# Kernel optimization log

Measured on AMD Instinct MI355X. Metric: run time of the kernel, lower is better.

The kernel has to match this reference:

```python
import jax, jax.numpy as jnp
import numpy as np

BATCH, T, N = 8, 2048, 512


def setup_inputs() -> dict:
    key = jax.random.key(0)
    ks = jax.random.split(key, 8)
    scale = 1.0 / np.sqrt(2.0 * (N + N) / 2.0) / np.sqrt(2.0)  # GlorotNormal / sqrt(2)
    u = jax.random.normal(ks[0], (BATCH, T, N), dtype=jnp.float32)
    C_re = jax.random.normal(ks[1], (N, N), dtype=jnp.float32) * scale
    C_im = jax.random.normal(ks[2], (N, N), dtype=jnp.float32) * scale
    B_re = jax.random.normal(ks[3], (N, N), dtype=jnp.float32) * scale
    B_im = jax.random.normal(ks[4], (N, N), dtype=jnp.float32) * scale
    D = jax.random.normal(ks[5], (N,), dtype=jnp.float32)
    # nu drawn from the numerically-stable end of [log(-log rmax), log(-log rmin)]
    nu = jax.random.uniform(ks[6], (N,), minval=-4.6, maxval=-3.7, dtype=jnp.float32)
    theta = jax.random.uniform(ks[7], (N,), minval=0.0, maxval=3.14 / 10, dtype=jnp.float32)
    # gamma initialized as sqrt(1 - |lambda|^2), lambda = exp(-exp(nu) + i*theta)
    gamma = jnp.sqrt(1.0 - jnp.exp(-2.0 * jnp.exp(nu)))
    return {"u": u, "C_re": C_re, "C_im": C_im, "B_re": B_re, "B_im": B_im,
            "D": D, "nu": nu, "theta": theta, "gamma": gamma}


def reference(u, C_re, C_im, B_re, B_im, D, nu, theta, gamma):
    # log_lambda = -exp(nu) + i*theta  (the TF code names this `lambda_`)
    log_lam = (-jnp.exp(nu)).astype(jnp.complex64) + 1j * theta.astype(jnp.complex64)  # (n,)
    t = jnp.arange(u.shape[1], dtype=jnp.float32).astype(jnp.complex64)[:, None]       # (T,1)
    lam_pow = jnp.exp(log_lam[None, :] * t)    # (T,n) == diag(Lambda^t)
    lam_minpow = jnp.exp(-log_lam[None, :] * t)  # (T,n) == diag(Lambda^-t)
    Bm = (B_re + 1j * B_im).astype(jnp.complex64)  # (n,n)
    Cm = (C_re + 1j * C_im).astype(jnp.complex64)  # (n,n)
    # new_u = (gamma * u) @ B   (complex)
    new_u = (gamma * u).astype(jnp.complex64) @ Bm  # (b,t,n)
    # diag einsums in the original are elementwise multiplies
    x = jnp.cumsum(new_u * lam_minpow[None], axis=1) * lam_pow[None]  # (b,t,n)
    y = jnp.real(x @ Cm) + D * u
    return y
```

## Files before the change

kernel.cpp:

```cpp
#include <hip/hip_runtime.h>
#include <hip/hip_bf16.h>
#include <math.h>
#include <stdint.h>

#define BATCH 8
#define T_LEN 2048
#define NDIM 512
#define M_ROWS (BATCH * T_LEN)
#define CHUNK 32
#define NCHUNK (T_LEN / CHUNK)


typedef __attribute__((ext_vector_type(8))) short bf16x8;
typedef __attribute__((ext_vector_type(4))) float floatx4;

__device__ __forceinline__ unsigned short f2bf(float f) {
    union { float f; unsigned u; } v; v.f = f;
    unsigned r = v.u + 0x7fff + ((v.u >> 16) & 1);
    return (unsigned short)(r >> 16);
}
__device__ __forceinline__ float bf2f(unsigned short h) {
    union { unsigned u; float f; } v; v.u = ((unsigned)h) << 16;
    return v.f;
}
__device__ __forceinline__ float bf2f_lo(unsigned u) {
    union { unsigned u; float f; } v; v.u = u << 16; return v.f;
}
__device__ __forceinline__ float bf2f_hi(unsigned u) {
    union { unsigned u; float f; } v; v.u = u & 0xffff0000u; return v.f;
}

__device__ __forceinline__ void gld_lds16(const unsigned short* g, unsigned short* l) {
    __builtin_amdgcn_global_load_lds(
        (const __attribute__((address_space(1))) unsigned int*)(uintptr_t)g,
        (__attribute__((address_space(3))) unsigned int*)(uintptr_t)l,
        16, 0, 0);
}

__global__ __launch_bounds__(256) void k_prep(
    const float* __restrict__ u,
    const float* __restrict__ Bre, const float* __restrict__ Bim,
    const float* __restrict__ Cre, const float* __restrict__ Cim,
    const float* __restrict__ gamma,
    unsigned short* __restrict__ ubf,
    unsigned short* __restrict__ BT, unsigned short* __restrict__ CT)
{
    __shared__ unsigned short tile[32][33];
    const int blk = blockIdx.x;
    if (blk < 4096) {
        size_t i = ((size_t)blk * 256 + threadIdx.x) * 8;
        float4 a = *(const float4*)&u[i];
        float4 b = *(const float4*)&u[i + 4];
        ushort4 p0, p1;
        p0.x = f2bf(a.x); p0.y = f2bf(a.y); p0.z = f2bf(a.z); p0.w = f2bf(a.w);
        p1.x = f2bf(b.x); p1.y = f2bf(b.y); p1.z = f2bf(b.z); p1.w = f2bf(b.w);
        *(ushort4*)&ubf[i] = p0;
        *(ushort4*)&ubf[i + 4] = p1;
        return;
    }
    const int p = blk - 4096;
    const int z = p >> 8;
    const int rem = p & 255;
    const int n0 = (rem & 15) * 32, k0 = (rem >> 4) * 32;
    const float* __restrict__ src = (z == 0) ? Bre : (z == 1) ? Bim : (z == 2) ? Cre : Cim;
    const int tx = threadIdx.x & 31, ty = threadIdx.x >> 5;

#pragma unroll
    for (int j = 0; j < 4; ++j) {
        int k = k0 + ty + j * 8;
        float s = (z < 2) ? gamma[k] : (z == 3 ? -1.f : 1.f);
        tile[ty + j * 8][tx] = f2bf(s * src[(size_t)k * NDIM + n0 + tx]);
    }
    __syncthreads();
#pragma unroll
    for (int j = 0; j < 4; ++j) {
        int n = n0 + ty + j * 8;
        unsigned short v = tile[tx][ty + j * 8];
        if (z == 0) {
            int row = ((n >> 6) << 7) + (n & 63);
            BT[(size_t)row * 512 + k0 + tx] = v;
        } else if (z == 1) {
            int row = ((n >> 6) << 7) + 64 + (n & 63);
            BT[(size_t)row * 512 + k0 + tx] = v;
        } else if (z == 2) {
            int k = k0 + tx;
            int col = ((k >> 6) << 7) + (k & 63);
            CT[(size_t)n * 1024 + col] = v;
        } else {
            int k = k0 + tx;
            int col = ((k >> 6) << 7) + 64 + (k & 63);
            CT[(size_t)n * 1024 + col] = v;
        }
    }
}

__global__ __launch_bounds__(256) void k_gemm_in(
    const unsigned short* __restrict__ A,
    const unsigned short* __restrict__ BT,
    const float* __restrict__ nu, const float* __restrict__ theta,
    unsigned short* __restrict__ X,
    float* __restrict__ carry)
{
    __shared__ unsigned short smem[16384];
    unsigned short* const As0 = smem;
    unsigned short* const As1 = smem + 4096;
    unsigned short* const Bs0 = smem + 8192;
    unsigned short* const Bs1 = smem + 12288;

    const int tid = threadIdx.x;
    const int w = tid >> 6, l = tid & 63;
    const int bm = blockIdx.x * 128;
    const int bn = blockIdx.y * 128;
    const int wm = (w & 1) * 64, wn = (w >> 1) * 64;
    const int lm = l & 15, lq = l >> 4;
    const int srow = w * 16 + (l >> 2);
    const int scol = (l & 3) * 8;

    floatx4 acc[4][4];
#pragma unroll
    for (int i = 0; i < 4; ++i)
#pragma unroll
        for (int j = 0; j < 4; ++j) acc[i][j] = (floatx4)0.f;

    auto STAGE = [&](unsigned short* as, unsigned short* bs, int k0) {
        gld_lds16(&A[(size_t)(bm + srow) * 512 + k0 + scol],       &as[srow * 32 + scol]);
        gld_lds16(&A[(size_t)(bm + 64 + srow) * 512 + k0 + scol],  &as[(64 + srow) * 32 + scol]);
        gld_lds16(&BT[(size_t)(bn + srow) * 512 + k0 + scol],      &bs[srow * 32 + scol]);
        gld_lds16(&BT[(size_t)(bn + 64 + srow) * 512 + k0 + scol], &bs[(64 + srow) * 32 + scol]);
    };
    auto COMPUTE = [&](const unsigned short* as, const unsigned short* bs) {
        bf16x8 af[4], bfr[4];
#pragma unroll
        for (int i = 0; i < 4; ++i)
            af[i] = *(const bf16x8*)&as[(wm + i * 16 + lm) * 32 + lq * 8];
#pragma unroll
        for (int j = 0; j < 4; ++j)
            bfr[j] = *(const bf16x8*)&bs[(wn + j * 16 + lm) * 32 + lq * 8];
#pragma unroll
        for (int i = 0; i < 4; ++i)
#pragma unroll
            for (int j = 0; j < 4; ++j)
                acc[i][j] = __builtin_amdgcn_mfma_f32_16x16x32_bf16(af[i], bfr[j], acc[i][j], 0, 0, 0);
    };

    STAGE(As0, Bs0, 0);
    __syncthreads();
#pragma unroll
    for (int k0 = 0; k0 < 512; k0 += 64) {
        if (k0 + 32 < 512) STAGE(As1, Bs1, k0 + 32);
        COMPUTE(As0, Bs0);
        __syncthreads();
        if (k0 + 64 < 512) STAGE(As0, Bs0, k0 + 64);
        COMPUTE(As1, Bs1);
        __syncthreads();
    }

#pragma unroll
    for (int i = 0; i < 4; ++i)
#pragma unroll
        for (int j = 0; j < 4; ++j) {
            int col = wn + j * 16 + lm;
#pragma unroll
            for (int r = 0; r < 4; ++r) {
                int row = wm + i * 16 + lq * 4 + r;
                unsigned short v = f2bf(acc[i][j][r]);
                smem[row * 128 + col] = v;
                X[(size_t)(bm + row) * 1024 + bn + col] = v;
            }
        }
    __syncthreads();
    {
        const int chunk = tid >> 6;
        const int ch = tid & 63;
        const int n = (bn >> 1) + ch;
        const float rr = __expf(-__expf(nu[n]));
        const float lre = rr * __cosf(theta[n]);
        const float lim = rr * __sinf(theta[n]);
        const unsigned short* base = &smem[chunk * 32 * 128 + ch];
        float xre = 0.f, xim = 0.f;
#pragma unroll 8
        for (int t = 0; t < 32; ++t) {
            float ure = bf2f(base[t * 128]);
            float uim = bf2f(base[t * 128 + 64]);
            float a = lre * xre - lim * xim + ure;
            float b = lre * xim + lim * xre + uim;
            xre = a; xim = b;
        }
        const int bb = bm >> 11;
        const int cg = ((bm & 2047) >> 5) + chunk;
        size_t ci = ((size_t)bb * NCHUNK + cg) * NDIM + n;
        *(float2*)&carry[ci * 2] = make_float2(xre, xim);
    }
}

__global__ __launch_bounds__(256) void k_scan_apply(
    unsigned short* __restrict__ X,
    const float* __restrict__ nu, const float* __restrict__ theta,
    const float* __restrict__ carry)
{
    const int t2 = threadIdx.x;
    const int n0 = 2 * t2;
    const int b = blockIdx.x >> 6, c = blockIdx.x & 63;
    const float ex0 = __expf(nu[n0]), ex1 = __expf(nu[n0 + 1]);
    const float r0 = __expf(-ex0), r1 = __expf(-ex1);
    const float lre0 = r0 * __cosf(theta[n0]),     lim0 = r0 * __sinf(theta[n0]);
    const float lre1 = r1 * __cosf(theta[n0 + 1]), lim1 = r1 * __sinf(theta[n0 + 1]);
    const float rc0 = expf(-ex0 * (float)CHUNK), rc1 = expf(-ex1 * (float)CHUNK);
    const float th0 = theta[n0] * (float)CHUNK,  th1 = theta[n0 + 1] * (float)CHUNK;
    const float A0 = rc0 * cosf(th0), B0 = rc0 * sinf(th0);
    const float A1 = rc1 * cosf(th1), B1 = rc1 * sinf(th1);

    float xre0 = 0.f, xim0 = 0.f, xre1 = 0.f, xim1 = 0.f;
    for (int cc = 0; cc < c; ++cc) {
        size_t idx = ((size_t)b * NCHUNK + cc) * NDIM + n0;
        float4 cv = *(const float4*)&carry[idx * 2];
        float a0 = A0 * xre0 - B0 * xim0 + cv.x;
        float b0 = A0 * xim0 + B0 * xre0 + cv.y;
        float a1 = A1 * xre1 - B1 * xim1 + cv.z;
        float b1 = A1 * xim1 + B1 * xre1 + cv.w;
        xre0 = a0; xim0 = b0; xre1 = a1; xim1 = b1;
    }

    const int recol = ((n0 >> 6) << 7) + (n0 & 63);
    size_t m = (size_t)b * T_LEN + (size_t)c * CHUNK;
#pragma unroll 8
    for (int t = 0; t < CHUNK; ++t, ++m) {
        unsigned re = *(const unsigned*)&X[m * 1024 + recol];
        unsigned im = *(const unsigned*)&X[m * 1024 + recol + 64];
        float u0 = bf2f_lo(re), u1 = bf2f_hi(re);
        float v0 = bf2f_lo(im), v1 = bf2f_hi(im);
        float a0 = lre0 * xre0 - lim0 * xim0 + u0;
        float b0 = lre0 * xim0 + lim0 * xre0 + v0;
        float a1 = lre1 * xre1 - lim1 * xim1 + u1;
        float b1 = lre1 * xim1 + lim1 * xre1 + v1;
        xre0 = a0; xim0 = b0; xre1 = a1; xim1 = b1;
        unsigned pr = (unsigned)f2bf(xre0) | ((unsigned)f2bf(xre1) << 16);
        unsigned pim = (unsigned)f2bf(xim0) | ((unsigned)f2bf(xim1) << 16);
        *(unsigned*)&X[m * 1024 + recol] = pr;
        *(unsigned*)&X[m * 1024 + recol + 64] = pim;
    }
}

__global__ __launch_bounds__(256) void k_gemm_out(
    const unsigned short* __restrict__ Xbf,
    const unsigned short* __restrict__ CT,
    const float* __restrict__ D,
    const unsigned short* __restrict__ Ubf,
    float* __restrict__ Y)
{
    __shared__ unsigned short smem[16384];
    unsigned short* const As0 = smem;
    unsigned short* const As1 = smem + 4096;
    unsigned short* const Bs0 = smem + 8192;
    unsigned short* const Bs1 = smem + 12288;

    const int tid = threadIdx.x;
    const int w = tid >> 6, l = tid & 63;
    const int bm = blockIdx.x * 128;
    const int bn = blockIdx.y * 128;
    const int wm = (w & 1) * 64, wn = (w >> 1) * 64;
    const int lm = l & 15, lq = l >> 4;
    const int srow = w * 16 + (l >> 2);
    const int scol = (l & 3) * 8;

    floatx4 acc[4][4];
#pragma unroll
    for (int i = 0; i < 4; ++i)
#pragma unroll
        for (int j = 0; j < 4; ++j) acc[i][j] = (floatx4)0.f;

    auto STAGE = [&](unsigned short* as, unsigned short* bs, int k0) {
        gld_lds16(&Xbf[(size_t)(bm + srow) * 1024 + k0 + scol],      &as[srow * 32 + scol]);
        gld_lds16(&Xbf[(size_t)(bm + 64 + srow) * 1024 + k0 + scol], &as[(64 + srow) * 32 + scol]);
        gld_lds16(&CT[(size_t)(bn + srow) * 1024 + k0 + scol],       &bs[srow * 32 + scol]);
        gld_lds16(&CT[(size_t)(bn + 64 + srow) * 1024 + k0 + scol],  &bs[(64 + srow) * 32 + scol]);
    };
    auto COMPUTE = [&](const unsigned short* as, const unsigned short* bs) {
        bf16x8 af[4], bfr[4];
#pragma unroll
        for (int i = 0; i < 4; ++i)
            af[i] = *(const bf16x8*)&as[(wm + i * 16 + lm) * 32 + lq * 8];
#pragma unroll
        for (int j = 0; j < 4; ++j)
            bfr[j] = *(const bf16x8*)&bs[(wn + j * 16 + lm) * 32 + lq * 8];
#pragma unroll
        for (int i = 0; i < 4; ++i)
#pragma unroll
            for (int j = 0; j < 4; ++j)
                acc[i][j] = __builtin_amdgcn_mfma_f32_16x16x32_bf16(af[i], bfr[j], acc[i][j], 0, 0, 0);
    };

    STAGE(As0, Bs0, 0);
    __syncthreads();
#pragma unroll
    for (int k0 = 0; k0 < 1024; k0 += 64) {
        if (k0 + 32 < 1024) STAGE(As1, Bs1, k0 + 32);
        COMPUTE(As0, Bs0);
        __syncthreads();
        if (k0 + 64 < 1024) STAGE(As0, Bs0, k0 + 64);
        COMPUTE(As1, Bs1);
        __syncthreads();
    }

#pragma unroll
    for (int i = 0; i < 4; ++i)
#pragma unroll
        for (int j = 0; j < 4; ++j) {
            int col = bn + wn + j * 16 + lm;
            float dv = D[col];
#pragma unroll
            for (int r = 0; r < 4; ++r) {
                int row = bm + wm + i * 16 + lq * 4 + r;
                size_t off = (size_t)row * NDIM + col;
                Y[off] = acc[i][j][r] + dv * bf2f(Ubf[off]);
            }
        }
}

extern "C" void kernel_launch(void* const* d_in, const int* in_sizes, int n_in,
                              void* d_out, int out_size, void* d_ws, size_t ws_size,
                              hipStream_t stream)
{
    const float* u     = (const float*)d_in[0];
    const float* C_re  = (const float*)d_in[1];
    const float* C_im  = (const float*)d_in[2];
    const float* B_re  = (const float*)d_in[3];
    const float* B_im  = (const float*)d_in[4];
    const float* D     = (const float*)d_in[5];
    const float* nu    = (const float*)d_in[6];
    const float* theta = (const float*)d_in[7];
    const float* gamma = (const float*)d_in[8];
    float* y = (float*)d_out;

    unsigned short* X   = (unsigned short*)d_ws;
    unsigned short* ubf = X + (size_t)M_ROWS * 1024;
    unsigned short* BT  = ubf + (size_t)M_ROWS * 512;
    unsigned short* CT  = BT + (size_t)1024 * 512;
    float* carry = (float*)(CT + (size_t)512 * 1024);

    k_prep<<<4096 + 1024, 256, 0, stream>>>(u, B_re, B_im, C_re, C_im, gamma, ubf, BT, CT);
    k_gemm_in<<<dim3(M_ROWS / 128, 8), 256, 0, stream>>>(ubf, BT, nu, theta, X, carry);
    k_scan_apply<<<BATCH * NCHUNK, 256, 0, stream>>>(X, nu, theta, carry);
    k_gemm_out<<<dim3(M_ROWS / 128, 4), 256, 0, stream>>>(X, CT, D, ubf, y);
}
```

Baseline: 181.5 us.

## Deepen GEMM LDS pipelines to triple/quad buffering with explicit vmcnt waits

Both GEMM kernels move from double-buffered LDS staging with full __syncthreads to a multi-stage prefetch ring: three buffers in the input GEMM and four in the output GEMM. Explicit s_waitcnt vmcnt counts let several global-to-LDS loads stay in flight while MFMA work runs on an older buffer. Raw s_barrier calls and sched_barrier fences control ordering. The goal is to hide global memory latency better, at the cost of more LDS per block, which may lower occupancy, and fragile hand-tuned wait counts.

```diff
diff --git a/kernel.cpp b/kernel.cpp
--- a/kernel.cpp
+++ b/kernel.cpp
@@ -13,6 +13,8 @@
 
 typedef __attribute__((ext_vector_type(8))) short bf16x8;
 typedef __attribute__((ext_vector_type(4))) float floatx4;
+
+#define VMWAIT(n) asm volatile("s_waitcnt vmcnt(" #n ")" ::: "memory")
 
 __device__ __forceinline__ unsigned short f2bf(float f) {
     union { float f; unsigned u; } v; v.f = f;
@@ -101,11 +103,7 @@
     unsigned short* __restrict__ X,
     float* __restrict__ carry)
 {
-    __shared__ unsigned short smem[16384];
-    unsigned short* const As0 = smem;
-    unsigned short* const As1 = smem + 4096;
-    unsigned short* const Bs0 = smem + 8192;
-    unsigned short* const Bs1 = smem + 12288;
+    __shared__ unsigned short smem[24576];
 
     const int tid = threadIdx.x;
     const int w = tid >> 6, l = tid & 63;
@@ -122,13 +120,18 @@
 #pragma unroll
         for (int j = 0; j < 4; ++j) acc[i][j] = (floatx4)0.f;
 
-    auto STAGE = [&](unsigned short* as, unsigned short* bs, int k0) {
+    auto STAGE = [&](int buf, int t) {
+        unsigned short* as = &smem[buf * 8192];
+        unsigned short* bs = as + 4096;
+        const int k0 = t * 32;
         gld_lds16(&A[(size_t)(bm + srow) * 512 + k0 + scol],       &as[srow * 32 + scol]);
         gld_lds16(&A[(size_t)(bm + 64 + srow) * 512 + k0 + scol],  &as[(64 + srow) * 32 + scol]);
         gld_lds16(&BT[(size_t)(bn + srow) * 512 + k0 + scol],      &bs[srow * 32 + scol]);
         gld_lds16(&BT[(size_t)(bn + 64 + srow) * 512 + k0 + scol], &bs[(64 + srow) * 32 + scol]);
     };
-    auto COMPUTE = [&](const unsigned short* as, const unsigned short* bs) {
+    auto COMPUTE = [&](int buf) {
+        const unsigned short* as = &smem[buf * 8192];
+        const unsigned short* bs = as + 4096;
         bf16x8 af[4], bfr[4];
 #pragma unroll
         for (int i = 0; i < 4; ++i)
@@ -143,18 +146,30 @@
                 acc[i][j] = __builtin_amdgcn_mfma_f32_16x16x32_bf16(af[i], bfr[j], acc[i][j], 0, 0, 0);
     };
 
-    STAGE(As0, Bs0, 0);
+    STAGE(0, 0);
+    STAGE(1, 1);
+#pragma unroll
+    for (int t = 0; t < 14; ++t) {
+        STAGE((t + 2) % 3, t + 2);
+        VMWAIT(8);
+        __builtin_amdgcn_s_barrier();
+        __builtin_amdgcn_sched_barrier(0);
+        COMPUTE(t % 3);
+        __builtin_amdgcn_sched_barrier(0);
+        __builtin_amdgcn_s_barrier();
+    }
+    VMWAIT(4);
+    __builtin_amdgcn_s_barrier();
+    __builtin_amdgcn_sched_barrier(0);
+    COMPUTE(2);
+    __builtin_amdgcn_sched_barrier(0);
+    __builtin_amdgcn_s_barrier();
+    VMWAIT(0);
+    __builtin_amdgcn_s_barrier();
+    __builtin_amdgcn_sched_barrier(0);
+    COMPUTE(0);
+
     __syncthreads();
-#pragma unroll
-    for (int k0 = 0; k0 < 512; k0 += 64) {
-        if (k0 + 32 < 512) STAGE(As1, Bs1, k0 + 32);
-        COMPUTE(As0, Bs0);
-        __syncthreads();
-        if (k0 + 64 < 512) STAGE(As0, Bs0, k0 + 64);
-        COMPUTE(As1, Bs1);
-        __syncthreads();
-    }
-
 #pragma unroll
     for (int i = 0; i < 4; ++i)
 #pragma unroll
@@ -248,11 +263,7 @@
     const unsigned short* __restrict__ Ubf,
     float* __restrict__ Y)
 {
-    __shared__ unsigned short smem[16384];
-    unsigned short* const As0 = smem;
-    unsigned short* const As1 = smem + 4096;
-    unsigned short* const Bs0 = smem + 8192;
-    unsigned short* const Bs1 = smem + 12288;
+    __shared__ unsigned short smem[32768];
 
     const int tid = threadIdx.x;
     const int w = tid >> 6, l = tid & 63;
@@ -269,13 +280,18 @@
 #pragma unroll
         for (int j = 0; j < 4; ++j) acc[i][j] = (floatx4)0.f;
 
-    auto STAGE = [&](unsigned short* as, unsigned short* bs, int k0) {
+    auto STAGE = [&](int buf, int t) {
+        unsigned short* as = &smem[buf * 8192];
+        unsigned short* bs = as + 4096;
+        const int k0 = t * 32;
         gld_lds16(&Xbf[(size_t)(bm + srow) * 1024 + k0 + scol],      &as[srow * 32 + scol]);
         gld_lds16(&Xbf[(size_t)(bm + 64 + srow) * 1024 + k0 + scol], &as[(64 + srow) * 32 + scol]);
         gld_lds16(&CT[(size_t)(bn + srow) * 1024 + k0 + scol],       &bs[srow * 32 + scol]);
         gld_lds16(&CT[(size_t)(bn + 64 + srow) * 1024 + k0 + scol],  &bs[(64 + srow) * 32 + scol]);
     };
-    auto COMPUTE = [&](const unsigned short* as, const unsigned short* bs) {
+    auto COMPUTE = [&](int buf) {
+        const unsigned short* as = &smem[buf * 8192];
+        const unsigned short* bs = as + 4096;
         bf16x8 af[4], bfr[4];
 #pragma unroll
         for (int i = 0; i < 4; ++i)
@@ -290,17 +306,35 @@
                 acc[i][j] = __builtin_amdgcn_mfma_f32_16x16x32_bf16(af[i], bfr[j], acc[i][j], 0, 0, 0);
     };
 
-    STAGE(As0, Bs0, 0);
-    __syncthreads();
-#pragma unroll
-    for (int k0 = 0; k0 < 1024; k0 += 64) {
-        if (k0 + 32 < 1024) STAGE(As1, Bs1, k0 + 32);
-        COMPUTE(As0, Bs0);
-        __syncthreads();
-        if (k0 + 64 < 1024) STAGE(As0, Bs0, k0 + 64);
-        COMPUTE(As1, Bs1);
-        __syncthreads();
-    }
+    STAGE(0, 0);
+    STAGE(1, 1);
+    STAGE(2, 2);
+#pragma unroll
+    for (int t = 0; t < 29; ++t) {
+        STAGE((t + 3) & 3, t + 3);
+        VMWAIT(12);
+        __builtin_amdgcn_s_barrier();
+        __builtin_amdgcn_sched_barrier(0);
+        COMPUTE(t & 3);
+        __builtin_amdgcn_sched_barrier(0);
+        __builtin_amdgcn_s_barrier();
+    }
+    VMWAIT(8);
+    __builtin_amdgcn_s_barrier();
+    __builtin_amdgcn_sched_barrier(0);
+    COMPUTE(1);
+    __builtin_amdgcn_sched_barrier(0);
+    __builtin_amdgcn_s_barrier();
+    VMWAIT(4);
+    __builtin_amdgcn_s_barrier();
+    __builtin_amdgcn_sched_barrier(0);
+    COMPUTE(2);
+    __builtin_amdgcn_sched_barrier(0);
+    __builtin_amdgcn_s_barrier();
+    VMWAIT(0);
+    __builtin_amdgcn_s_barrier();
+    __builtin_amdgcn_sched_barrier(0);
+    COMPUTE(3);
 
 #pragma unroll
     for (int i = 0; i < 4; ++i)
```

Measured after the change: 172.6 us. 1.05x faster.
